# Kernel optimization log

Measured on AMD Instinct MI355X. Metric: run time of the kernel, lower is better.

Reference implementation:

```python
import jax, jax.numpy as jnp
import numpy as np

N_NODES = 50000
N_GROUPS = 512
D_FEAT = 128
D_HID = 128
N_CLASS = 16
NEG_SLOPE = 0.2


def gat_conv(x, edge_index, W, a_src, a_dst, bias, n):
    """Single-head PyG-style GATConv (with self-loops, eval mode / no dropout)."""
    h = x @ W  # [n, D_HID]
    loop = jnp.arange(n)
    src = jnp.concatenate([edge_index[0], loop])  # neighbors j
    dst = jnp.concatenate([edge_index[1], loop])  # targets i
    a_s = h @ a_src  # [n]
    a_d = h @ a_dst  # [n]
    e = jax.nn.leaky_relu(a_s[src] + a_d[dst], NEG_SLOPE)  # [E+n]
    # segment softmax over incoming edges of each dst node
    m = jax.ops.segment_max(e, dst, num_segments=n)
    e = jnp.exp(e - m[dst])
    denom = jax.ops.segment_sum(e, dst, num_segments=n)
    alpha = e / denom[dst]
    out = jax.ops.segment_sum(alpha[:, None] * h[src], dst, num_segments=n)
    return out + bias


def setup_inputs() -> dict:
    key = jax.random.key(0)
    ks = jax.random.split(key, 12)
    s_f = 1.0 / np.sqrt(D_FEAT)
    s_h = 1.0 / np.sqrt(D_HID)
    return {
        "x_full": jax.random.normal(ks[0], (N_NODES, D_FEAT), jnp.float32),
        "x_group": jax.random.normal(ks[1], (N_GROUPS, D_FEAT), jnp.float32),
        "W_full": jax.random.normal(ks[2], (D_FEAT, D_HID), jnp.float32) * s_f,
        "a_src_full": jax.random.normal(ks[3], (D_HID,), jnp.float32) * s_h,
        "a_dst_full": jax.random.normal(ks[4], (D_HID,), jnp.float32) * s_h,
        "bias_full": jnp.zeros((D_HID,), jnp.float32),
        "W_group": jax.random.normal(ks[5], (D_FEAT, D_HID), jnp.float32) * s_f,
        "a_src_group": jax.random.normal(ks[6], (D_HID,), jnp.float32) * s_h,
        "a_dst_group": jax.random.normal(ks[7], (D_HID,), jnp.float32) * s_h,
        "bias_group": jnp.zeros((D_HID,), jnp.float32),
        "fc_W": jax.random.normal(ks[8], (D_HID, N_CLASS), jnp.float32) * s_h,
        "fc_b": jnp.zeros((N_CLASS,), jnp.float32),
        "edge_index_full": jax.random.randint(ks[9], (2, 600000), 0, N_NODES, jnp.int64),
        "edge_index_group": jax.random.randint(ks[10], (2, 4096), 0, N_GROUPS, jnp.int64),
        "node_group": jax.random.randint(ks[11], (N_NODES,), 0, N_GROUPS, jnp.int64),
    }


def reference(x_full, x_group, W_full, a_src_full, a_dst_full, bias_full,
              W_group, a_src_group, a_dst_group, bias_group, fc_W, fc_b,
              edge_index_full, edge_index_group, node_group):
    full_x = jax.nn.elu(gat_conv(x_full, edge_index_full, W_full, a_src_full,
                                 a_dst_full, bias_full, N_NODES))   # [N, D_HID]
    group_x = jax.nn.elu(gat_conv(x_group, edge_index_group, W_group, a_src_group,
                                  a_dst_group, bias_group, N_GROUPS))  # [G, D_HID]

    # mean feature of groups adjacent to each group (edges src->dst in group graph)
    gsrc, gdst = edge_index_group[0], edge_index_group[1]
    adj_sum = jax.ops.segment_sum(group_x[gdst], gsrc, num_segments=N_GROUPS)
    cnt = jax.ops.segment_sum(jnp.ones_like(gsrc, jnp.float32), gsrc, num_segments=N_GROUPS)
    adj_mean = adj_sum / jnp.maximum(cnt, 1.0)[:, None]  # [G, D_HID]

    gf = group_x[node_group]   # group feature per node, [N, D_HID]
    am = adj_mean[node_group]  # adjacent-group mean per node, [N, D_HID]

    # dot(node, group_feature) and mean_j dot(node, adj_j) == dot(node, adj_mean)
    iw_group = jnp.sum(full_x * gf, axis=-1, keepdims=True)  # [N, 1]
    iw_adj = jnp.sum(full_x * am, axis=-1, keepdims=True)    # [N, 1]

    updated = full_x + iw_group * gf + iw_adj * am  # [N, D_HID]
    out = updated @ fc_W + fc_b                     # [N, N_CLASS]
    return (out, updated)
```

## Files before the change

kernel.cpp:

```cpp
#include <hip/hip_runtime.h>

typedef unsigned short u16;
typedef unsigned int u32;

static __device__ __forceinline__ float lrelu(float x) { return x >= 0.f ? x : 0.2f * x; }

static __device__ __forceinline__ u16 f2bf(float f) {
    u32 u = __float_as_uint(f);
    u += 0x7FFF + ((u >> 16) & 1);
    return (u16)(u >> 16);
}
static __device__ __forceinline__ float bflo(u32 u) { return __uint_as_float(u << 16); }
static __device__ __forceinline__ float bfhi(u32 u) { return __uint_as_float(u & 0xffff0000u); }

static __device__ __forceinline__ float fc_reduce16(float f0, float f1, int lane,
                                                    const float4* __restrict__ fW4) {
    float4 w00 = fW4[(2 * lane) * 4 + 0], w01 = fW4[(2 * lane) * 4 + 1];
    float4 w02 = fW4[(2 * lane) * 4 + 2], w03 = fW4[(2 * lane) * 4 + 3];
    float4 w10 = fW4[(2 * lane + 1) * 4 + 0], w11 = fW4[(2 * lane + 1) * 4 + 1];
    float4 w12 = fW4[(2 * lane + 1) * 4 + 2], w13 = fW4[(2 * lane + 1) * 4 + 3];
    float4 q0, q1, q2, q3;
    q0.x = f0 * w00.x + f1 * w10.x; q0.y = f0 * w00.y + f1 * w10.y;
    q0.z = f0 * w00.z + f1 * w10.z; q0.w = f0 * w00.w + f1 * w10.w;
    q1.x = f0 * w01.x + f1 * w11.x; q1.y = f0 * w01.y + f1 * w11.y;
    q1.z = f0 * w01.z + f1 * w11.z; q1.w = f0 * w01.w + f1 * w11.w;
    q2.x = f0 * w02.x + f1 * w12.x; q2.y = f0 * w02.y + f1 * w12.y;
    q2.z = f0 * w02.z + f1 * w12.z; q2.w = f0 * w02.w + f1 * w12.w;
    q3.x = f0 * w03.x + f1 * w13.x; q3.y = f0 * w03.y + f1 * w13.y;
    q3.z = f0 * w03.z + f1 * w13.z; q3.w = f0 * w03.w + f1 * w13.w;
    bool h5 = (lane & 32) != 0, h4 = (lane & 16) != 0;
    bool h3 = (lane & 8) != 0, h2 = (lane & 4) != 0;
    float4 s0, s1, k0, k1;
    s0.x = h5 ? q0.x : q2.x; s0.y = h5 ? q0.y : q2.y;
    s0.z = h5 ? q0.z : q2.z; s0.w = h5 ? q0.w : q2.w;
    s1.x = h5 ? q1.x : q3.x; s1.y = h5 ? q1.y : q3.y;
    s1.z = h5 ? q1.z : q3.z; s1.w = h5 ? q1.w : q3.w;
    s0.x = __shfl_xor(s0.x, 32); s0.y = __shfl_xor(s0.y, 32);
    s0.z = __shfl_xor(s0.z, 32); s0.w = __shfl_xor(s0.w, 32);
    s1.x = __shfl_xor(s1.x, 32); s1.y = __shfl_xor(s1.y, 32);
    s1.z = __shfl_xor(s1.z, 32); s1.w = __shfl_xor(s1.w, 32);
    k0.x = h5 ? q2.x : q0.x; k0.y = h5 ? q2.y : q0.y;
    k0.z = h5 ? q2.z : q0.z; k0.w = h5 ? q2.w : q0.w;
    k1.x = h5 ? q3.x : q1.x; k1.y = h5 ? q3.y : q1.y;
    k1.z = h5 ? q3.z : q1.z; k1.w = h5 ? q3.w : q1.w;
    float4 a0, a1;
    a0.x = k0.x + s0.x; a0.y = k0.y + s0.y; a0.z = k0.z + s0.z; a0.w = k0.w + s0.w;
    a1.x = k1.x + s1.x; a1.y = k1.y + s1.y; a1.z = k1.z + s1.z; a1.w = k1.w + s1.w;
    float4 sB, kB;
    sB.x = h4 ? a0.x : a1.x; sB.y = h4 ? a0.y : a1.y;
    sB.z = h4 ? a0.z : a1.z; sB.w = h4 ? a0.w : a1.w;
    sB.x = __shfl_xor(sB.x, 16); sB.y = __shfl_xor(sB.y, 16);
    sB.z = __shfl_xor(sB.z, 16); sB.w = __shfl_xor(sB.w, 16);
    kB.x = h4 ? a1.x : a0.x; kB.y = h4 ? a1.y : a0.y;
    kB.z = h4 ? a1.z : a0.z; kB.w = h4 ? a1.w : a0.w;
    float4 b;
    b.x = kB.x + sB.x; b.y = kB.y + sB.y; b.z = kB.z + sB.z; b.w = kB.w + sB.w;
    float sCx = h3 ? b.x : b.z, sCy = h3 ? b.y : b.w;
    sCx = __shfl_xor(sCx, 8); sCy = __shfl_xor(sCy, 8);
    float kCx = h3 ? b.z : b.x, kCy = h3 ? b.w : b.y;
    float c2x = kCx + sCx, c2y = kCy + sCy;
    float sD = h2 ? c2x : c2y;
    sD = __shfl_xor(sD, 4);
    float kD = h2 ? c2y : c2x;
    float r = kD + sD;
    r += __shfl_xor(r, 1);
    r += __shfl_xor(r, 2);
    return r;
}

__global__ __launch_bounds__(256) void gemm_both_kernel(
        const float* __restrict__ Xf, const float* __restrict__ Wf,
        const float* __restrict__ asf, const float* __restrict__ adf,
        u16* __restrict__ Hbf, float* __restrict__ as_f, float* __restrict__ ad_f, int N,
        const float* __restrict__ Xg, const float* __restrict__ Wg,
        const float* __restrict__ asg, const float* __restrict__ adg,
        u16* __restrict__ Hbg, float* __restrict__ as_g, float* __restrict__ ad_g, int G,
        int nbFull) {
    const float* X; const float* W; const float* av; const float* dv;
    u16* Hb; float* as_out; float* ad_out; int n_lim; long base;
    if (blockIdx.x < nbFull) {
        X = Xf; W = Wf; av = asf; dv = adf; Hb = Hbf; as_out = as_f; ad_out = ad_f;
        n_lim = N; base = (long)blockIdx.x * 32;
    } else {
        X = Xg; W = Wg; av = asg; dv = adg; Hb = Hbg; as_out = as_g; ad_out = ad_g;
        n_lim = G; base = (long)(blockIdx.x - nbFull) * 32;
    }
    __shared__ float Ws[64 * 128];
    __shared__ float Xs[32 * 128];
    int tid = threadIdx.x;
    float4* Ws4 = (float4*)Ws;
    float4* Xs4 = (float4*)Xs;
    const float4* X4 = (const float4*)(X + base * 128);
    for (int i = tid; i < 1024; i += 256) {
        int r = i >> 5;
        Xs4[i] = (base + r < n_lim) ? X4[i] : make_float4(0.f, 0.f, 0.f, 0.f);
    }
    int fgrp = tid & 31;
    int n0 = (tid >> 5) * 4;
    float4 acc[4] = {};
    for (int half = 0; half < 2; ++half) {
        __syncthreads();
        const float4* W4 = (const float4*)(W + half * 64 * 128);
        for (int i = tid; i < 2048; i += 256) Ws4[i] = W4[i];
        __syncthreads();
        #pragma unroll 4
        for (int kk = 0; kk < 64; ++kk) {
            float4 w = Ws4[kk * 32 + fgrp];
            #pragma unroll
            for (int j = 0; j < 4; ++j) {
                float x = Xs[(n0 + j) * 128 + half * 64 + kk];
                acc[j].x += x * w.x; acc[j].y += x * w.y;
                acc[j].z += x * w.z; acc[j].w += x * w.w;
            }
        }
    }
    float4 as4 = ((const float4*)av)[fgrp];
    float4 ad4 = ((const float4*)dv)[fgrp];
    float ps[4], pd[4];
    #pragma unroll
    for (int j = 0; j < 4; ++j) {
        ps[j] = acc[j].x * as4.x + acc[j].y * as4.y + acc[j].z * as4.z + acc[j].w * as4.w;
        pd[j] = acc[j].x * ad4.x + acc[j].y * ad4.y + acc[j].z * ad4.z + acc[j].w * ad4.w;
    }
    #pragma unroll
    for (int off = 16; off; off >>= 1) {
        #pragma unroll
        for (int j = 0; j < 4; ++j) {
            ps[j] += __shfl_xor(ps[j], off);
            pd[j] += __shfl_xor(pd[j], off);
        }
    }
    if ((tid & 31) == 0) {
        #pragma unroll
        for (int j = 0; j < 4; ++j) {
            long n = base + n0 + j;
            if (n < n_lim) { as_out[n] = ps[j]; ad_out[n] = pd[j]; }
        }
    }
    #pragma unroll
    for (int j = 0; j < 4; ++j) {
        long n = base + n0 + j;
        if (n < n_lim) {
            ushort4 hv;
            hv.x = f2bf(acc[j].x); hv.y = f2bf(acc[j].y);
            hv.z = f2bf(acc[j].z); hv.w = f2bf(acc[j].w);
            ((ushort4*)(Hb + n * 128))[fgrp] = hv;
        }
    }
}

__global__ __launch_bounds__(256) void hist2_kernel(const int* __restrict__ efd, int E, int N,
                                                    const int* __restrict__ egd, int Eg, int G,
                                                    int Npad, int* __restrict__ deg) {
    int i = blockIdx.x * 256 + threadIdx.x;
    int totF = E + N;
    int tot = totF + Eg + G;
    if (i >= tot) return;
    int d;
    if (i < E) d = efd[i];
    else if (i < totF) d = i - E;
    else {
        int j = i - totF;
        d = Npad + ((j < Eg) ? egd[j] : (j - Eg));
    }
    atomicAdd(&deg[d], 1);
}

__global__ __launch_bounds__(256) void scan1_kernel(const int* __restrict__ deg, int n,
                                                    int* __restrict__ bsum) {
    __shared__ int s[256];
    int i = blockIdx.x * 256 + threadIdx.x;
    s[threadIdx.x] = (i < n) ? deg[i] : 0;
    __syncthreads();
    for (int off = 128; off; off >>= 1) {
        if (threadIdx.x < off) s[threadIdx.x] += s[threadIdx.x + off];
        __syncthreads();
    }
    if (threadIdx.x == 0) bsum[blockIdx.x] = s[0];
}

__global__ __launch_bounds__(256) void scan3_kernel(int* __restrict__ deg, int n, int nb,
                                                    const int* __restrict__ bsum,
                                                    int* __restrict__ offs, int Ltot) {
    __shared__ int sb[256];
    __shared__ int s[256];
    int t = threadIdx.x;
    sb[t] = (t < nb) ? bsum[t] : 0;
    __syncthreads();
    for (int off = 1; off < 256; off <<= 1) {
        int u = (t >= off) ? sb[t - off] : 0;
        __syncthreads();
        sb[t] += u;
        __syncthreads();
    }
    int blockOff = (blockIdx.x == 0) ? 0 : sb[blockIdx.x - 1];
    if (blockIdx.x == 0 && t == 0) offs[Ltot] = sb[nb - 1];

    int i = blockIdx.x * 256 + t;
    int v = (i < n) ? deg[i] : 0;
    s[t] = v;
    __syncthreads();
    for (int off = 1; off < 256; off <<= 1) {
        int u = (t >= off) ? s[t - off] : 0;
        __syncthreads();
        s[t] += u;
        __syncthreads();
    }
    if (i < n) {
        int excl = s[t] - v + blockOff;
        offs[i] = excl;
        deg[i] = excl;
    }
}

__global__ __launch_bounds__(256) void place2_kernel(const int* __restrict__ efs,
                                                     const int* __restrict__ efd, int E, int N,
                                                     const int* __restrict__ egs,
                                                     const int* __restrict__ egd, int Eg, int G,
                                                     int Npad,
                                                     const float* __restrict__ a_s,
                                                     const float* __restrict__ a_d,
                                                     const float* __restrict__ a_sg,
                                                     const float* __restrict__ a_dg,
                                                     int* __restrict__ cursor,
                                                     int2* __restrict__ sepack) {
    int i = blockIdx.x * 256 + threadIdx.x;
    int totF = E + N;
    int tot = totF + Eg + G;
    if (i >= tot) return;
    int s, d, dcur;
    float av;
    if (i < totF) {
        if (i < E) { s = efs[i]; d = efd[i]; } else { s = d = i - E; }
        av = a_s[s] + a_d[d];
        dcur = d;
    } else {
        int j = i - totF;
        if (j < Eg) { s = egs[j]; d = egd[j]; } else { s = d = j - Eg; }
        av = a_sg[s] + a_dg[d];
        dcur = Npad + d;
    }
    float e = expf(lrelu(av));
    int pos = atomicAdd(&cursor[dcur], 1);
    sepack[pos] = make_int2(s, __float_as_int(e));
}

__global__ __launch_bounds__(256) void pull2_kernel(const u16* __restrict__ Hf,
                                                    const u16* __restrict__ Hg,
                                                    const int* __restrict__ offs,
                                                    const int2* __restrict__ sepack,
                                                    const float* __restrict__ bias_f,
                                                    const float* __restrict__ bias_g,
                                                    float* __restrict__ fx,
                                                    float* __restrict__ gx,
                                                    int N, int G, int Npad) {
    int gid = blockIdx.x * 256 + threadIdx.x;
    int w = gid >> 6, lane = gid & 63;
    const u16* H;
    const float* bias;
    float* out;
    int idx;
    if (w < N) {
        H = Hf; bias = bias_f; out = fx + (long)w * 128; idx = w;
    } else if (w < N + G) {
        int g = w - N;
        H = Hg; bias = bias_g; out = gx + (long)g * 128; idx = Npad + g;
    } else return;
    int beg = offs[idx], end = offs[idx + 1];
    const uint4* H16 = (const uint4*)H;
    int sub = lane >> 4;
    int fc = lane & 15;
    float a0 = 0.f, a1 = 0.f, a2 = 0.f, a3 = 0.f;
    float a4 = 0.f, a5 = 0.f, a6 = 0.f, a7 = 0.f;
    float ss = 0.f;
    for (int b = beg; b < end; b += 64) {
        int m = end - b;
        if (m > 64) m = 64;
        int2 se = (lane < m) ? sepack[b + lane] : make_int2(0, 0);
        int sl = se.x;
        float el = __int_as_float(se.y);
        int kend = (m + 3) & ~3;
        int k = 0;
        for (; k + 8 <= kend; k += 8) {
            int s0 = __shfl(sl, k + sub);
            float e0 = __shfl(el, k + sub);
            int s1 = __shfl(sl, k + 4 + sub);
            float e1 = __shfl(el, k + 4 + sub);
            uint4 h0 = H16[(long)s0 * 16 + fc];
            uint4 h1 = H16[(long)s1 * 16 + fc];
            a0 += e0 * bflo(h0.x); a1 += e0 * bfhi(h0.x);
            a2 += e0 * bflo(h0.y); a3 += e0 * bfhi(h0.y);
            a4 += e0 * bflo(h0.z); a5 += e0 * bfhi(h0.z);
            a6 += e0 * bflo(h0.w); a7 += e0 * bfhi(h0.w);
            a0 += e1 * bflo(h1.x); a1 += e1 * bfhi(h1.x);
            a2 += e1 * bflo(h1.y); a3 += e1 * bfhi(h1.y);
            a4 += e1 * bflo(h1.z); a5 += e1 * bfhi(h1.z);
            a6 += e1 * bflo(h1.w); a7 += e1 * bfhi(h1.w);
            ss += e0 + e1;
        }
        if (k < kend) {
            int s0 = __shfl(sl, k + sub);
            float e0 = __shfl(el, k + sub);
            uint4 h0 = H16[(long)s0 * 16 + fc];
            a0 += e0 * bflo(h0.x); a1 += e0 * bfhi(h0.x);
            a2 += e0 * bflo(h0.y); a3 += e0 * bfhi(h0.y);
            a4 += e0 * bflo(h0.z); a5 += e0 * bfhi(h0.z);
            a6 += e0 * bflo(h0.w); a7 += e0 * bfhi(h0.w);
            ss += e0;
        }
    }
    a0 += __shfl_xor(a0, 16); a0 += __shfl_xor(a0, 32);
    a1 += __shfl_xor(a1, 16); a1 += __shfl_xor(a1, 32);
    a2 += __shfl_xor(a2, 16); a2 += __shfl_xor(a2, 32);
    a3 += __shfl_xor(a3, 16); a3 += __shfl_xor(a3, 32);
    a4 += __shfl_xor(a4, 16); a4 += __shfl_xor(a4, 32);
    a5 += __shfl_xor(a5, 16); a5 += __shfl_xor(a5, 32);
    a6 += __shfl_xor(a6, 16); a6 += __shfl_xor(a6, 32);
    a7 += __shfl_xor(a7, 16); a7 += __shfl_xor(a7, 32);
    ss += __shfl_xor(ss, 16); ss += __shfl_xor(ss, 32);
    if (lane < 16) {
        float inv = 1.f / ss;
        const float4* b4 = (const float4*)bias;
        float4 bA = b4[lane * 2], bB = b4[lane * 2 + 1];
        float4 oA, oB;
        oA.x = a0 * inv + bA.x; oA.y = a1 * inv + bA.y;
        oA.z = a2 * inv + bA.z; oA.w = a3 * inv + bA.w;
        oB.x = a4 * inv + bB.x; oB.y = a5 * inv + bB.y;
        oB.z = a6 * inv + bB.z; oB.w = a7 * inv + bB.w;
        oA.x = oA.x > 0.f ? oA.x : expm1f(oA.x);
        oA.y = oA.y > 0.f ? oA.y : expm1f(oA.y);
        oA.z = oA.z > 0.f ? oA.z : expm1f(oA.z);
        oA.w = oA.w > 0.f ? oA.w : expm1f(oA.w);
        oB.x = oB.x > 0.f ? oB.x : expm1f(oB.x);
        oB.y = oB.y > 0.f ? oB.y : expm1f(oB.y);
        oB.z = oB.z > 0.f ? oB.z : expm1f(oB.z);
        oB.w = oB.w > 0.f ? oB.w : expm1f(oB.w);
        float4* o4 = (float4*)out;
        o4[lane * 2] = oA;
        o4[lane * 2 + 1] = oB;
    }
}

__global__ __launch_bounds__(256) void adj_kernel(const int* __restrict__ gsrc,
                                                  const int* __restrict__ gdst, int Eg,
                                                  const float* __restrict__ gx,
                                                  float* __restrict__ adj_sum,
                                                  float* __restrict__ cnt) {
    int gid = blockIdx.x * 256 + threadIdx.x;
    int i = gid >> 6, lane = gid & 63;
    if (i >= Eg) return;
    int s = gsrc[i], d = gdst[i];
    float2 gv = ((const float2*)gx)[(long)d * 64 + lane];
    atomicAdd(&adj_sum[(long)s * 128 + 2 * lane], gv.x);
    atomicAdd(&adj_sum[(long)s * 128 + 2 * lane + 1], gv.y);
    if (lane == 0) atomicAdd(&cnt[s], 1.f);
}

__global__ __launch_bounds__(256) void final3_kernel(const int* __restrict__ node_group,
                                                     const float* __restrict__ gx,
                                                     const float* __restrict__ adj_sum,
                                                     const float* __restrict__ cnt,
                                                     const float* __restrict__ fcW,
                                                     const float* __restrict__ fcb,
                                                     float* __restrict__ upd,
                                                     float* __restrict__ out, int N) {
    int gid = blockIdx.x * 256 + threadIdx.x;
    int n = gid >> 6, lane = gid & 63;
    if (n >= N) return;
    int g = node_group[n];
    float2 row = ((const float2*)upd)[(long)n * 64 + lane];
    float2 gf = ((const float2*)gx)[(long)g * 64 + lane];
    float inv_cnt = 1.f / fmaxf(cnt[g], 1.f);
    float2 as2 = ((const float2*)adj_sum)[(long)g * 64 + lane];
    float amx = as2.x * inv_cnt, amy = as2.y * inv_cnt;
    float pg = row.x * gf.x + row.y * gf.y;
    float pa = row.x * amx + row.y * amy;
    #pragma unroll
    for (int off = 32; off; off >>= 1) {
        pg += __shfl_xor(pg, off);
        pa += __shfl_xor(pa, off);
    }
    float ux = row.x + pg * gf.x + pa * amx;
    float uy = row.y + pg * gf.y + pa * amy;
    ((float2*)upd)[(long)n * 64 + lane] = make_float2(ux, uy);
    float r = fc_reduce16(ux, uy, lane, (const float4*)fcW);
    int cls = (lane >> 2) & 15;
    if ((lane & 3) == 0) out[(long)n * 16 + cls] = r + fcb[cls];
}

extern "C" void kernel_launch(void* const* d_in, const int* in_sizes, int n_in,
                              void* d_out, int out_size, void* d_ws, size_t ws_size,
                              hipStream_t stream) {
    const float* x_full = (const float*)d_in[0];
    const float* x_group = (const float*)d_in[1];
    const float* W_full = (const float*)d_in[2];
    const float* a_src_full = (const float*)d_in[3];
    const float* a_dst_full = (const float*)d_in[4];
    const float* bias_full = (const float*)d_in[5];
    const float* W_group = (const float*)d_in[6];
    const float* a_src_g = (const float*)d_in[7];
    const float* a_dst_g = (const float*)d_in[8];
    const float* bias_g = (const float*)d_in[9];
    const float* fc_W = (const float*)d_in[10];
    const float* fc_b = (const float*)d_in[11];
    const int* ef = (const int*)d_in[12];
    const int* eg = (const int*)d_in[13];
    const int* node_group = (const int*)d_in[14];

    int N = in_sizes[0] / 128;
    int G = in_sizes[1] / 128;
    int E = in_sizes[12] / 2;
    int Eg = in_sizes[13] / 2;
    const int* ef_src = ef;
    const int* ef_dst = ef + E;
    const int* eg_src = eg;
    const int* eg_dst = eg + Eg;

    int Npad = (N + 255) & ~255;
    int Ltot = Npad + G;
    int LtotPad = (Ltot + 255) & ~255;
    int totF = E + N;
    int tot = totF + Eg + G;

    float* out_cls = (float*)d_out;
    float* fx = out_cls + (long)N * 16;

    char* w = (char*)d_ws;
    auto alloc = [&](size_t bytes) {
        char* p = w;
        w += (bytes + 255) & ~(size_t)255;
        return p;
    };
    u16* h_full = (u16*)alloc((size_t)N * 128 * 2);
    u16* h_g = (u16*)alloc((size_t)G * 128 * 2);
    float* a_s = (float*)alloc((size_t)N * 4);
    float* a_d = (float*)alloc((size_t)N * 4);
    float* a_sg = (float*)alloc((size_t)G * 4);
    float* a_dg = (float*)alloc((size_t)G * 4);
    float* gx = (float*)alloc((size_t)G * 128 * 4);
    float* adj_sum = (float*)alloc((size_t)G * 128 * 4);
    float* cnt = (float*)alloc((size_t)G * 4);
    int* deg = (int*)alloc((size_t)LtotPad * 4);
    int* offs = (int*)alloc((size_t)(LtotPad + 1) * 4);
    int2* sepack = (int2*)alloc((size_t)tot * 8);
    int* bsum = (int*)alloc(256 * 4);

    size_t zero_span = (char*)(deg + LtotPad) - (char*)adj_sum;
    (void)hipMemsetAsync(adj_sum, 0, zero_span, stream);

    auto cdiv = [](int a, int b) { return (a + b - 1) / b; };

    int nbFull = cdiv(N, 32);
    gemm_both_kernel<<<nbFull + cdiv(G, 32), 256, 0, stream>>>(
        x_full, W_full, a_src_full, a_dst_full, h_full, a_s, a_d, N,
        x_group, W_group, a_src_g, a_dst_g, h_g, a_sg, a_dg, G, nbFull);

    int nb = cdiv(Ltot, 256);
    hist2_kernel<<<cdiv(tot, 256), 256, 0, stream>>>(ef_dst, E, N, eg_dst, Eg, G, Npad, deg);
    scan1_kernel<<<nb, 256, 0, stream>>>(deg, Ltot, bsum);
    scan3_kernel<<<nb, 256, 0, stream>>>(deg, Ltot, nb, bsum, offs, Ltot);
    place2_kernel<<<cdiv(tot, 256), 256, 0, stream>>>(ef_src, ef_dst, E, N, eg_src, eg_dst,
                                                      Eg, G, Npad, a_s, a_d, a_sg, a_dg,
                                                      deg, sepack);

    pull2_kernel<<<cdiv((N + G) * 64, 256), 256, 0, stream>>>(h_full, h_g, offs, sepack,
                                                              bias_full, bias_g,
                                                              fx, gx, N, G, Npad);

    adj_kernel<<<cdiv(Eg * 64, 256), 256, 0, stream>>>(eg_src, eg_dst, Eg, gx, adj_sum, cnt);
    final3_kernel<<<cdiv(N * 64, 256), 256, 0, stream>>>(node_group, gx, adj_sum, cnt,
                                                         fc_W, fc_b, fx, out_cls, N);
}
```

Baseline: 295.6 us.

## Distribute fc layer linearly over update terms and fuse histogram into GEMM launch

Uses linearity of the final fc layer: out = fx·W + pg·(gf·W) + pa·(am·W) + b. fx·W is computed in the pull kernel while the row is still in registers, and the per-group products gf·W and am·W are precomputed in a new small group kernel. The final kernel then does a 16-wide combine instead of a 128x16 reduction per node. It also merges the degree histogram into the GEMM launch as extra blocks, removing one launch and letting the two overlap. The costs are an extra small kernel, extra fxW/adj_mean buffers and more register pressure in the pull kernel.

```diff
diff --git a/kernel.cpp b/kernel.cpp
--- a/kernel.cpp
+++ b/kernel.cpp
@@ -68,14 +68,34 @@
     return r;
 }
 
-__global__ __launch_bounds__(256) void gemm_both_kernel(
+__global__ __launch_bounds__(256) void gemm_hist_kernel(
         const float* __restrict__ Xf, const float* __restrict__ Wf,
         const float* __restrict__ asf, const float* __restrict__ adf,
         u16* __restrict__ Hbf, float* __restrict__ as_f, float* __restrict__ ad_f, int N,
         const float* __restrict__ Xg, const float* __restrict__ Wg,
         const float* __restrict__ asg, const float* __restrict__ adg,
         u16* __restrict__ Hbg, float* __restrict__ as_g, float* __restrict__ ad_g, int G,
-        int nbFull) {
+        int nbFull, int nbGemm,
+        const int* __restrict__ efd, int E, const int* __restrict__ egd, int Eg,
+        int Npad, int* __restrict__ deg) {
+    __shared__ float Ws[64 * 128];
+    __shared__ float Xs[32 * 128];
+    int tid = threadIdx.x;
+    if (blockIdx.x >= nbGemm) {
+        int i = (blockIdx.x - nbGemm) * 256 + tid;
+        int totF = E + N;
+        int tot = totF + Eg + G;
+        if (i >= tot) return;
+        int d;
+        if (i < E) d = efd[i];
+        else if (i < totF) d = i - E;
+        else {
+            int j = i - totF;
+            d = Npad + ((j < Eg) ? egd[j] : (j - Eg));
+        }
+        atomicAdd(&deg[d], 1);
+        return;
+    }
     const float* X; const float* W; const float* av; const float* dv;
     u16* Hb; float* as_out; float* ad_out; int n_lim; long base;
     if (blockIdx.x < nbFull) {
@@ -85,9 +105,6 @@
         X = Xg; W = Wg; av = asg; dv = adg; Hb = Hbg; as_out = as_g; ad_out = ad_g;
         n_lim = G; base = (long)(blockIdx.x - nbFull) * 32;
     }
-    __shared__ float Ws[64 * 128];
-    __shared__ float Xs[32 * 128];
-    int tid = threadIdx.x;
     float4* Ws4 = (float4*)Ws;
     float4* Xs4 = (float4*)Xs;
     const float4* X4 = (const float4*)(X + base * 128);
@@ -147,23 +164,6 @@
             ((ushort4*)(Hb + n * 128))[fgrp] = hv;
         }
     }
-}
-
-__global__ __launch_bounds__(256) void hist2_kernel(const int* __restrict__ efd, int E, int N,
-                                                    const int* __restrict__ egd, int Eg, int G,
-                                                    int Npad, int* __restrict__ deg) {
-    int i = blockIdx.x * 256 + threadIdx.x;
-    int totF = E + N;
-    int tot = totF + Eg + G;
-    if (i >= tot) return;
-    int d;
-    if (i < E) d = efd[i];
-    else if (i < totF) d = i - E;
-    else {
-        int j = i - totF;
-        d = Npad + ((j < Eg) ? egd[j] : (j - Eg));
-    }
-    atomicAdd(&deg[d], 1);
 }
 
 __global__ __launch_bounds__(256) void scan1_kernel(const int* __restrict__ deg, int n,
@@ -251,8 +251,10 @@
                                                     const int2* __restrict__ sepack,
                                                     const float* __restrict__ bias_f,
                                                     const float* __restrict__ bias_g,
+                                                    const float* __restrict__ fcW,
                                                     float* __restrict__ fx,
                                                     float* __restrict__ gx,
+                                                    float* __restrict__ fxW,
                                                     int N, int G, int Npad) {
     int gid = blockIdx.x * 256 + threadIdx.x;
     int w = gid >> 6, lane = gid & 63;
@@ -260,7 +262,8 @@
     const float* bias;
     float* out;
     int idx;
-    if (w < N) {
+    bool isFull = (w < N);
+    if (isFull) {
         H = Hf; bias = bias_f; out = fx + (long)w * 128; idx = w;
     } else if (w < N + G) {
         int g = w - N;
@@ -318,26 +321,44 @@
     a6 += __shfl_xor(a6, 16); a6 += __shfl_xor(a6, 32);
     a7 += __shfl_xor(a7, 16); a7 += __shfl_xor(a7, 32);
     ss += __shfl_xor(ss, 16); ss += __shfl_xor(ss, 32);
-    if (lane < 16) {
-        float inv = 1.f / ss;
-        const float4* b4 = (const float4*)bias;
-        float4 bA = b4[lane * 2], bB = b4[lane * 2 + 1];
-        float4 oA, oB;
-        oA.x = a0 * inv + bA.x; oA.y = a1 * inv + bA.y;
-        oA.z = a2 * inv + bA.z; oA.w = a3 * inv + bA.w;
-        oB.x = a4 * inv + bB.x; oB.y = a5 * inv + bB.y;
-        oB.z = a6 * inv + bB.z; oB.w = a7 * inv + bB.w;
-        oA.x = oA.x > 0.f ? oA.x : expm1f(oA.x);
-        oA.y = oA.y > 0.f ? oA.y : expm1f(oA.y);
-        oA.z = oA.z > 0.f ? oA.z : expm1f(oA.z);
-        oA.w = oA.w > 0.f ? oA.w : expm1f(oA.w);
-        oB.x = oB.x > 0.f ? oB.x : expm1f(oB.x);
-        oB.y = oB.y > 0.f ? oB.y : expm1f(oB.y);
-        oB.z = oB.z > 0.f ? oB.z : expm1f(oB.z);
-        oB.w = oB.w > 0.f ? oB.w : expm1f(oB.w);
-        float4* o4 = (float4*)out;
-        o4[lane * 2] = oA;
-        o4[lane * 2 + 1] = oB;
+    float inv = 1.f / ss;
+    const float4* b4 = (const float4*)bias;
+    float4 bA = b4[fc * 2], bB = b4[fc * 2 + 1];
+    float o0 = a0 * inv + bA.x, o1 = a1 * inv + bA.y;
+    float o2 = a2 * inv + bA.z, o3 = a3 * inv + bA.w;
+    float o4 = a4 * inv + bB.x, o5 = a5 * inv + bB.y;
+    float o6 = a6 * inv + bB.z, o7 = a7 * inv + bB.w;
+    o0 = o0 > 0.f ? o0 : expm1f(o0); o1 = o1 > 0.f ? o1 : expm1f(o1);
+    o2 = o2 > 0.f ? o2 : expm1f(o2); o3 = o3 > 0.f ? o3 : expm1f(o3);
+    o4 = o4 > 0.f ? o4 : expm1f(o4); o5 = o5 > 0.f ? o5 : expm1f(o5);
+    o6 = o6 > 0.f ? o6 : expm1f(o6); o7 = o7 > 0.f ? o7 : expm1f(o7);
+    if (sub == 0) {
+        float4* o4p = (float4*)out;
+        o4p[fc * 2] = make_float4(o0, o1, o2, o3);
+        o4p[fc * 2 + 1] = make_float4(o4, o5, o6, o7);
+    }
+    if (isFull) {
+        const float4* fW4 = (const float4*)fcW;
+        int rb = (8 * fc) * 4 + sub;
+        float4 w0 = fW4[rb], w1 = fW4[rb + 4], w2 = fW4[rb + 8], w3 = fW4[rb + 12];
+        float4 w4 = fW4[rb + 16], w5 = fW4[rb + 20], w6 = fW4[rb + 24], w7 = fW4[rb + 28];
+        float4 p;
+        p.x = o0 * w0.x + o1 * w1.x + o2 * w2.x + o3 * w3.x +
+              o4 * w4.x + o5 * w5.x + o6 * w6.x + o7 * w7.x;
+        p.y = o0 * w0.y + o1 * w1.y + o2 * w2.y + o3 * w3.y +
+              o4 * w4.y + o5 * w5.y + o6 * w6.y + o7 * w7.y;
+        p.z = o0 * w0.z + o1 * w1.z + o2 * w2.z + o3 * w3.z +
+              o4 * w4.z + o5 * w5.z + o6 * w6.z + o7 * w7.z;
+        p.w = o0 * w0.w + o1 * w1.w + o2 * w2.w + o3 * w3.w +
+              o4 * w4.w + o5 * w5.w + o6 * w6.w + o7 * w7.w;
+        #pragma unroll
+        for (int mask = 8; mask; mask >>= 1) {
+            p.x += __shfl_xor(p.x, mask);
+            p.y += __shfl_xor(p.y, mask);
+            p.z += __shfl_xor(p.z, mask);
+            p.w += __shfl_xor(p.w, mask);
+        }
+        if (fc == 0) ((float4*)(fxW + (long)w * 16))[sub] = p;
     }
 }
 
@@ -356,11 +377,37 @@
     if (lane == 0) atomicAdd(&cnt[s], 1.f);
 }
 
+__global__ __launch_bounds__(256) void groupfc_kernel(const float* __restrict__ gx,
+                                                      const float* __restrict__ adj_sum,
+                                                      const float* __restrict__ cnt,
+                                                      const float* __restrict__ fcW,
+                                                      float* __restrict__ adj_mean,
+                                                      float* __restrict__ gfW,
+                                                      float* __restrict__ amW, int G) {
+    int gid = blockIdx.x * 256 + threadIdx.x;
+    int g = gid >> 6, lane = gid & 63;
+    if (g >= G) return;
+    float inv = 1.f / fmaxf(cnt[g], 1.f);
+    float2 as2 = ((const float2*)adj_sum)[(long)g * 64 + lane];
+    float2 am = make_float2(as2.x * inv, as2.y * inv);
+    ((float2*)adj_mean)[(long)g * 64 + lane] = am;
+    float2 gf = ((const float2*)gx)[(long)g * 64 + lane];
+    const float4* fW4 = (const float4*)fcW;
+    float rg = fc_reduce16(gf.x, gf.y, lane, fW4);
+    float ra = fc_reduce16(am.x, am.y, lane, fW4);
+    int cls = (lane >> 2) & 15;
+    if ((lane & 3) == 0) {
+        gfW[(long)g * 16 + cls] = rg;
+        amW[(long)g * 16 + cls] = ra;
+    }
+}
+
 __global__ __launch_bounds__(256) void final3_kernel(const int* __restrict__ node_group,
                                                      const float* __restrict__ gx,
-                                                     const float* __restrict__ adj_sum,
-                                                     const float* __restrict__ cnt,
-                                                     const float* __restrict__ fcW,
+                                                     const float* __restrict__ adj_mean,
+                                                     const float* __restrict__ gfW,
+                                                     const float* __restrict__ amW,
+                                                     const float* __restrict__ fxW,
                                                      const float* __restrict__ fcb,
                                                      float* __restrict__ upd,
                                                      float* __restrict__ out, int N) {
@@ -370,22 +417,21 @@
     int g = node_group[n];
     float2 row = ((const float2*)upd)[(long)n * 64 + lane];
     float2 gf = ((const float2*)gx)[(long)g * 64 + lane];
-    float inv_cnt = 1.f / fmaxf(cnt[g], 1.f);
-    float2 as2 = ((const float2*)adj_sum)[(long)g * 64 + lane];
-    float amx = as2.x * inv_cnt, amy = as2.y * inv_cnt;
+    float2 am = ((const float2*)adj_mean)[(long)g * 64 + lane];
     float pg = row.x * gf.x + row.y * gf.y;
-    float pa = row.x * amx + row.y * amy;
+    float pa = row.x * am.x + row.y * am.y;
     #pragma unroll
     for (int off = 32; off; off >>= 1) {
         pg += __shfl_xor(pg, off);
         pa += __shfl_xor(pa, off);
     }
-    float ux = row.x + pg * gf.x + pa * amx;
-    float uy = row.y + pg * gf.y + pa * amy;
+    float ux = row.x + pg * gf.x + pa * am.x;
+    float uy = row.y + pg * gf.y + pa * am.y;
     ((float2*)upd)[(long)n * 64 + lane] = make_float2(ux, uy);
-    float r = fc_reduce16(ux, uy, lane, (const float4*)fcW);
-    int cls = (lane >> 2) & 15;
-    if ((lane & 3) == 0) out[(long)n * 16 + cls] = r + fcb[cls];
+    if (lane < 16) {
+        out[(long)n * 16 + lane] = fxW[(long)n * 16 + lane] + pg * gfW[(long)g * 16 + lane] +
+                                   pa * amW[(long)g * 16 + lane] + fcb[lane];
+    }
 }
 
 extern "C" void kernel_launch(void* const* d_in, const int* in_sizes, int n_in,
@@ -438,6 +484,10 @@
     float* a_sg = (float*)alloc((size_t)G * 4);
     float* a_dg = (float*)alloc((size_t)G * 4);
     float* gx = (float*)alloc((size_t)G * 128 * 4);
+    float* adj_mean = (float*)alloc((size_t)G * 128 * 4);
+    float* fxW = (float*)alloc((size_t)N * 16 * 4);
+    float* gfW = (float*)alloc((size_t)G * 16 * 4);
+    float* amW = (float*)alloc((size_t)G * 16 * 4);
     float* adj_sum = (float*)alloc((size_t)G * 128 * 4);
     float* cnt = (float*)alloc((size_t)G * 4);
     int* deg = (int*)alloc((size_t)LtotPad * 4);
@@ -451,12 +501,14 @@
     auto cdiv = [](int a, int b) { return (a + b - 1) / b; };
 
     int nbFull = cdiv(N, 32);
-    gemm_both_kernel<<<nbFull + cdiv(G, 32), 256, 0, stream>>>(
+    int nbGemm = nbFull + cdiv(G, 32);
+    int nbHist = cdiv(tot, 256);
+    gemm_hist_kernel<<<nbGemm + nbHist, 256, 0, stream>>>(
         x_full, W_full, a_src_full, a_dst_full, h_full, a_s, a_d, N,
-        x_group, W_group, a_src_g, a_dst_g, h_g, a_sg, a_dg, G, nbFull);
+        x_group, W_group, a_src_g, a_dst_g, h_g, a_sg, a_dg, G,
+        nbFull, nbGemm, ef_dst, E, eg_dst, Eg, Npad, deg);
 
     int nb = cdiv(Ltot, 256);
-    hist2_kernel<<<cdiv(tot, 256), 256, 0, stream>>>(ef_dst, E, N, eg_dst, Eg, G, Npad, deg);
     scan1_kernel<<<nb, 256, 0, stream>>>(deg, Ltot, bsum);
     scan3_kernel<<<nb, 256, 0, stream>>>(deg, Ltot, nb, bsum, offs, Ltot);
     place2_kernel<<<cdiv(tot, 256), 256, 0, stream>>>(ef_src, ef_dst, E, N, eg_src, eg_dst,
@@ -464,10 +516,12 @@
                                                       deg, sepack);
 
     pull2_kernel<<<cdiv((N + G) * 64, 256), 256, 0, stream>>>(h_full, h_g, offs, sepack,
-                                                              bias_full, bias_g,
-                                                              fx, gx, N, G, Npad);
+                                                              bias_full, bias_g, fc_W,
+                                                              fx, gx, fxW, N, G, Npad);
 
     adj_kernel<<<cdiv(Eg * 64, 256), 256, 0, stream>>>(eg_src, eg_dst, Eg, gx, adj_sum, cnt);
-    final3_kernel<<<cdiv(N * 64, 256), 256, 0, stream>>>(node_group, gx, adj_sum, cnt,
-                                                         fc_W, fc_b, fx, out_cls, N);
-}
+    groupfc_kernel<<<cdiv(G * 64, 256), 256, 0, stream>>>(gx, adj_sum, cnt, fc_W,
+                                                          adj_mean, gfW, amW, G);
+    final3_kernel<<<cdiv(N * 64, 256), 256, 0, stream>>>(node_group, gx, adj_mean, gfW, amW,
+                                                         fxW, fc_b, fx, out_cls, N);
+}
```

Measured after the change: 282.5 us. 1.05x faster.
